# Performance work log

Hardware: AMD Instinct MI355X
Metric: run time of the kernel (lower is better)

## Reference

```python
import jax, jax.numpy as jnp
import numpy as np

B, T, S, D, H, E, K, FF = 4, 1024, 1024, 1024, 16, 8, 2, 4096
DH = D // H
EPS = 1e-5

def layernorm(x, g, b):
    m = x.mean(-1, keepdims=True)
    v = x.var(-1, keepdims=True)
    return (x - m) / jnp.sqrt(v + EPS) * g + b

def mha(q, k, v, mask, wq, bq, wk, bk, wv, bv, wo, bo):
    Bq, Tq, _ = q.shape
    Tk = k.shape[1]
    Q = (q @ wq + bq).reshape(Bq, Tq, H, DH).transpose(0, 2, 1, 3)
    Kh = (k @ wk + bk).reshape(Bq, Tk, H, DH).transpose(0, 2, 1, 3)
    V = (v @ wv + bv).reshape(Bq, Tk, H, DH).transpose(0, 2, 1, 3)
    scores = jnp.einsum('bhqd,bhkd->bhqk', Q, Kh) / (DH ** 0.5)
    scores = jnp.where(mask != 0, scores, jnp.float32(-1e9))
    A = jax.nn.softmax(scores, axis=-1)
    O = jnp.einsum('bhqk,bhkd->bhqd', A, V).transpose(0, 2, 1, 3).reshape(Bq, Tq, D)
    return O @ wo + bo

def sparse_moe(x, wg, bg, w1, b1, w2, b2):
    # x: [B,T,D] -> tokens [N,D]
    Bx, Tx, _ = x.shape
    xt = x.reshape(-1, D)
    N = xt.shape[0]
    probs = jax.nn.softmax(xt @ wg + bg, axis=-1)          # [N,E]
    topv, topi = jax.lax.top_k(probs, K)                    # [N,K]
    topv = topv / topv.sum(-1, keepdims=True)
    gates = jnp.zeros((N, E), xt.dtype).at[jnp.arange(N)[:, None], topi].set(topv)
    h = jax.nn.relu(jnp.einsum('nd,edh->enh', xt, w1) + b1[:, None, :])  # [E,N,FF]
    y = jnp.einsum('enh,ehd->end', h, w2) + b2[:, None, :]               # [E,N,D]
    out = jnp.einsum('ne,end->nd', gates, y)
    return out.reshape(Bx, Tx, D)

def setup_inputs() -> dict:
    key = jax.random.key(0)
    ks = jax.random.split(key, 32)
    r = lambda k, s: jax.random.normal(k, s, dtype=jnp.float32) * 0.02
    inp = {
        'x': jax.random.normal(ks[0], (B, T, D), jnp.float32),
        'encoder_out': jax.random.normal(ks[1], (B, S, D), jnp.float32),
        'src_attn_mask': jnp.ones((B, 1, 1, S), jnp.int32),
        'tgt_attn_mask': jnp.tril(jnp.ones((T, T), jnp.int32))[None, None],
        'ln1_g': jnp.ones((D,), jnp.float32), 'ln1_b': jnp.zeros((D,), jnp.float32),
        'ln2_g': jnp.ones((D,), jnp.float32), 'ln2_b': jnp.zeros((D,), jnp.float32),
        'ln3_g': jnp.ones((D,), jnp.float32), 'ln3_b': jnp.zeros((D,), jnp.float32),
        'wq1': r(ks[2], (D, D)), 'bq1': jnp.zeros((D,), jnp.float32),
        'wk1': r(ks[3], (D, D)), 'bk1': jnp.zeros((D,), jnp.float32),
        'wv1': r(ks[4], (D, D)), 'bv1': jnp.zeros((D,), jnp.float32),
        'wo1': r(ks[5], (D, D)), 'bo1': jnp.zeros((D,), jnp.float32),
        'wq2': r(ks[6], (D, D)), 'bq2': jnp.zeros((D,), jnp.float32),
        'wk2': r(ks[7], (D, D)), 'bk2': jnp.zeros((D,), jnp.float32),
        'wv2': r(ks[8], (D, D)), 'bv2': jnp.zeros((D,), jnp.float32),
        'wo2': r(ks[9], (D, D)), 'bo2': jnp.zeros((D,), jnp.float32),
        'wg': r(ks[10], (D, E)), 'bg': jnp.zeros((E,), jnp.float32),
        'w1': r(ks[11], (E, D, FF)), 'b1': jnp.zeros((E, FF), jnp.float32),
        'w2': r(ks[12], (E, FF, D)), 'b2': jnp.zeros((E, D), jnp.float32),
    }
    return inp

def reference(x, encoder_out, src_attn_mask, tgt_attn_mask,
              ln1_g, ln1_b, ln2_g, ln2_b, ln3_g, ln3_b,
              wq1, bq1, wk1, bk1, wv1, bv1, wo1, bo1,
              wq2, bq2, wk2, bk2, wv2, bv2, wo2, bo2,
              wg, bg, w1, b1, w2, b2):
    # pre-norm residual: x + sublayer(LN(x)); dropout=0 (eval)
    n1 = layernorm(x, ln1_g, ln1_b)
    h1 = x + mha(n1, n1, n1, tgt_attn_mask, wq1, bq1, wk1, bk1, wv1, bv1, wo1, bo1)
    n2 = layernorm(h1, ln2_g, ln2_b)
    h2 = h1 + mha(n2, encoder_out, encoder_out, src_attn_mask, wq2, bq2, wk2, bk2, wv2, bv2, wo2, bo2)
    n3 = layernorm(h2, ln3_g, ln3_b)
    h3 = h2 + sparse_moe(n3, wg, bg, w1, b1, w2, b2)
    return h3
```

## Files before the change

### kernel.cpp

```cpp
#include <hip/hip_runtime.h>

typedef unsigned short u16;
typedef float f32x4 __attribute__((ext_vector_type(4)));
typedef short s16x8 __attribute__((ext_vector_type(8)));
typedef u16   u16x4 __attribute__((ext_vector_type(4)));

#define DEV static __device__ __forceinline__

DEV u16 f2b(float f){
  unsigned u = __builtin_bit_cast(unsigned, f);
  u += 0x7fffu + ((u >> 16) & 1u);
  return (u16)(u >> 16);
}
DEV float b2f(u16 h){ unsigned u = ((unsigned)h) << 16; return __builtin_bit_cast(float, u); }
DEV void tsplit(float v, u16& hv, u16& lv){
  unsigned u = __builtin_bit_cast(unsigned, v);
  hv = (u16)(u >> 16);
  float rest = v - __builtin_bit_cast(float, u & 0xffff0000u);
  lv = (u16)(__builtin_bit_cast(unsigned, rest) >> 16);
}
DEV float fexp2(float x){ float r; asm("v_exp_f32 %0, %1" : "=v"(r) : "v"(x)); return r; }

DEV void glds16(const u16* g, u16* l){
  __builtin_amdgcn_global_load_lds(
      (const __attribute__((address_space(1))) void*)g,
      (__attribute__((address_space(3))) void*)l, 16, 0, 0);
}

DEV f32x4 mfma3(s16x8 ah, s16x8 al, s16x8 bh, s16x8 bl, f32x4 c){
  c = __builtin_amdgcn_mfma_f32_16x16x32_bf16(ah, bh, c, 0, 0, 0);
  c = __builtin_amdgcn_mfma_f32_16x16x32_bf16(ah, bl, c, 0, 0, 0);
  c = __builtin_amdgcn_mfma_f32_16x16x32_bf16(al, bh, c, 0, 0, 0);
  return c;
}

constexpr int TT = 1024, DM = 1024, NE = 8, FFD = 4096;
constexpr int NTOK = 4096;

struct Ptr8 { const float* p[8]; };

__global__ __launch_bounds__(256) void trans8_k(Ptr8 srcs, u16* __restrict__ dh, u16* __restrict__ dl){
  __shared__ float tl[64][65];
  const float* src = srcs.p[blockIdx.z];
  u16* dsth = dh + (size_t)blockIdx.z * 1024 * 1024;
  u16* dstl = dl + (size_t)blockIdx.z * 1024 * 1024;
  const int tid = threadIdx.x;
  const int r0 = blockIdx.y * 64, c0 = blockIdx.x * 64;
  const int ty = tid >> 4, tx = tid & 15;
#pragma unroll
  for (int i = 0; i < 4; i++){
    int row = ty + i * 16;
    f32x4 v = *(const f32x4*)&src[(size_t)(r0 + row) * 1024 + c0 + tx * 4];
#pragma unroll
    for (int j = 0; j < 4; j++) tl[row][tx * 4 + j] = v[j];
  }
  __syncthreads();
#pragma unroll
  for (int i = 0; i < 4; i++){
    int drow = ty + i * 16;
    u16x4 oh, ol;
#pragma unroll
    for (int j = 0; j < 4; j++){
      float v = tl[tx * 4 + j][drow];
      u16 hh, ll; tsplit(v, hh, ll);
      oh[j] = hh; ol[j] = ll;
    }
    *(u16x4*)&dsth[(size_t)(c0 + drow) * 1024 + r0 + tx * 4] = oh;
    *(u16x4*)&dstl[(size_t)(c0 + drow) * 1024 + r0 + tx * 4] = ol;
  }
}

__global__ __launch_bounds__(256) void transb_k(const float* __restrict__ src0, u16* __restrict__ dst0, int R, int C){
  __shared__ float tl[64][65];
  const float* src = src0 + (size_t)blockIdx.z * R * C;
  u16* dst = dst0 + (size_t)blockIdx.z * R * C;
  const int tid = threadIdx.x;
  const int r0 = blockIdx.y * 64, c0 = blockIdx.x * 64;
  const int ty = tid >> 4, tx = tid & 15;
#pragma unroll
  for (int i = 0; i < 4; i++){
    int row = ty + i * 16;
    f32x4 v = *(const f32x4*)&src[(size_t)(r0 + row) * C + c0 + tx * 4];
#pragma unroll
    for (int j = 0; j < 4; j++) tl[row][tx * 4 + j] = v[j];
  }
  __syncthreads();
#pragma unroll
  for (int i = 0; i < 4; i++){
    int drow = ty + i * 16;
    u16x4 o;
#pragma unroll
    for (int j = 0; j < 4; j++) o[j] = f2b(tl[tx * 4 + j][drow]);
    *(u16x4*)&dst[(size_t)(c0 + drow) * R + r0 + tx * 4] = o;
  }
}

__global__ __launch_bounds__(256) void split_k(const float* __restrict__ src,
                                               u16* __restrict__ dh, u16* __restrict__ dl, int n4){
  int i = blockIdx.x * 256 + threadIdx.x;
  if (i < n4){
    f32x4 v = *(const f32x4*)&src[(size_t)i * 4];
    u16x4 oh, ol;
#pragma unroll
    for (int j = 0; j < 4; j++){ u16 hh, ll; tsplit(v[j], hh, ll); oh[j] = hh; ol[j] = ll; }
    *(u16x4*)&dh[(size_t)i * 4] = oh;
    *(u16x4*)&dl[(size_t)i * 4] = ol;
  }
}

__global__ __launch_bounds__(256) void ln_k(const float* __restrict__ x, const float* __restrict__ g,
                                            const float* __restrict__ b,
                                            u16* __restrict__ outH, u16* __restrict__ outL){
  __shared__ float red[8];
  const int row = blockIdx.x, tid = threadIdx.x, l = tid & 63, wave = tid >> 6;
  f32x4 v = *(const f32x4*)&x[(size_t)row * DM + tid * 4];
  float s = v[0] + v[1] + v[2] + v[3];
  float sq = v[0]*v[0] + v[1]*v[1] + v[2]*v[2] + v[3]*v[3];
#pragma unroll
  for (int m = 1; m < 64; m <<= 1){ s += __shfl_xor(s, m); sq += __shfl_xor(sq, m); }
  if (l == 0){ red[wave] = s; red[4 + wave] = sq; }
  __syncthreads();
  float tot = red[0] + red[1] + red[2] + red[3];
  float totq = red[4] + red[5] + red[6] + red[7];
  float mean = tot * (1.0f / DM);
  float var = totq * (1.0f / DM) - mean * mean;
  float rstd = rsqrtf(var + 1e-5f);
  f32x4 gg = *(const f32x4*)&g[tid * 4];
  f32x4 bb = *(const f32x4*)&b[tid * 4];
  u16x4 oh, ol;
#pragma unroll
  for (int j = 0; j < 4; j++){
    float y = (v[j] - mean) * rstd * gg[j] + bb[j];
    u16 hh, ll; tsplit(y, hh, ll); oh[j] = hh; ol[j] = ll;
  }
  *(u16x4*)&outH[(size_t)row * DM + tid * 4] = oh;
  if (outL) *(u16x4*)&outL[(size_t)row * DM + tid * 4] = ol;
}

struct QKVArgs {
  const u16* ah[3]; const u16* al[3]; const float* bias[3];
};

__global__ __launch_bounds__(256) void gemm_qkv3_k(
    QKVArgs args, const u16* __restrict__ Bhp, const u16* __restrict__ Blp,
    u16* __restrict__ QH, u16* __restrict__ QL,
    u16* __restrict__ KH, u16* __restrict__ KL,
    u16* __restrict__ VTH, u16* __restrict__ VTL)
{
  constexpr int K = DM;
  __shared__ alignas(16) u16 LAh[128 * 32], LAl[128 * 32];
  __shared__ alignas(16) u16 LBh[64 * 32], LBl[64 * 32];
  const int tid = threadIdx.x, l = tid & 63, wave = tid >> 6;
  const int seg = blockIdx.z;
  const int m0 = blockIdx.y * 128, n0 = blockIdx.x * 64;
  const int r0 = tid >> 2, seg8 = (tid & 3) * 8;
  const u16* gAh = args.ah[seg] + (size_t)(m0 + r0) * K + seg8;
  const u16* gAl = args.al[seg] + (size_t)(m0 + r0) * K + seg8;
  const u16* gBh = Bhp + (size_t)(seg * 1024 + n0 + r0) * K + seg8;
  const u16* gBl = Blp + (size_t)(seg * 1024 + n0 + r0) * K + seg8;
  u16* wAh = &LAh[wave * 512]; u16* wAl = &LAl[wave * 512];
  u16* wBh = &LBh[wave * 512]; u16* wBl = &LBl[wave * 512];
  const size_t K64 = (size_t)64 * K;
  f32x4 acc[4][2];
#pragma unroll
  for (int i = 0; i < 4; i++)
#pragma unroll
    for (int j = 0; j < 2; j++) acc[i][j] = f32x4{0.f, 0.f, 0.f, 0.f};
  const int wm = (wave >> 1) * 64, wn = (wave & 1) * 32;
  for (int kt = 0; kt < K; kt += 32){
    __syncthreads();
    glds16(gAh + kt, wAh); glds16(gAh + kt + K64, wAh + 2048);
    glds16(gAl + kt, wAl); glds16(gAl + kt + K64, wAl + 2048);
    glds16(gBh + kt, wBh);
    glds16(gBl + kt, wBl);
    __syncthreads();
    s16x8 afh[4], afl[4], bfh[2], bfl[2];
#pragma unroll
    for (int i = 0; i < 4; i++){
      int ar = (wm + i * 16 + (l & 15)) * 32 + (l >> 4) * 8;
      afh[i] = *(const s16x8*)&LAh[ar];
      afl[i] = *(const s16x8*)&LAl[ar];
    }
#pragma unroll
    for (int j = 0; j < 2; j++){
      int br = (wn + j * 16 + (l & 15)) * 32 + (l >> 4) * 8;
      bfh[j] = *(const s16x8*)&LBh[br];
      bfl[j] = *(const s16x8*)&LBl[br];
    }
#pragma unroll
    for (int i = 0; i < 4; i++)
#pragma unroll
      for (int j = 0; j < 2; j++)
        acc[i][j] = mfma3(afh[i], afl[i], bfh[j], bfl[j], acc[i][j]);
  }
  const float* bp = args.bias[seg];
  u16* DH = (seg == 0) ? QH : KH;
  u16* DL = (seg == 0) ? QL : KL;
#pragma unroll
  for (int i = 0; i < 4; i++)
#pragma unroll
    for (int r = 0; r < 4; r++){
      int row = m0 + wm + i * 16 + (l >> 4) * 4 + r;
#pragma unroll
      for (int j = 0; j < 2; j++){
        int col = n0 + wn + j * 16 + (l & 15);
        float v = acc[i][j][r] + bp[col];
        u16 hv, lv; tsplit(v, hv, lv);
        if (seg == 2){
          int bb = row >> 10, tq = row & 1023, hh = col >> 6, dd = col & 63;
          size_t vi = ((size_t)((bb << 4) + hh) * 64 + dd) * 1024 + tq;
          VTH[vi] = hv; VTL[vi] = lv;
        } else {
          size_t idx = (size_t)row * 1024 + col;
          DH[idx] = hv; DL[idx] = lv;
        }
      }
    }
}

__global__ __launch_bounds__(256) void gemm_o64_k(
    const u16* __restrict__ Ahp, const u16* __restrict__ Alp,
    const u16* __restrict__ Bhp, const u16* __restrict__ Blp,
    const float* __restrict__ bias, const float* __restrict__ res,
    float* __restrict__ Cf)
{
  constexpr int K = DM;
  __shared__ alignas(16) u16 LAh[64 * 32], LAl[64 * 32];
  __shared__ alignas(16) u16 LBh[64 * 32], LBl[64 * 32];
  const int tid = threadIdx.x, l = tid & 63, wave = tid >> 6;
  const int m0 = blockIdx.y * 64, n0 = blockIdx.x * 64;
  const int rA = tid >> 2, seg8 = (tid & 3) * 8;
  const u16* gAh = Ahp + (size_t)(m0 + rA) * K + seg8;
  const u16* gAl = Alp + (size_t)(m0 + rA) * K + seg8;
  const u16* gBh = Bhp + (size_t)(n0 + rA) * K + seg8;
  const u16* gBl = Blp + (size_t)(n0 + rA) * K + seg8;
  u16* wAh = &LAh[wave * 512]; u16* wAl = &LAl[wave * 512];
  u16* wBh = &LBh[wave * 512]; u16* wBl = &LBl[wave * 512];
  f32x4 acc[2][2];
#pragma unroll
  for (int i = 0; i < 2; i++)
#pragma unroll
    for (int j = 0; j < 2; j++) acc[i][j] = f32x4{0.f, 0.f, 0.f, 0.f};
  const int wm = (wave >> 1) * 32, wn = (wave & 1) * 32;
  for (int kt = 0; kt < K; kt += 32){
    __syncthreads();
    glds16(gAh + kt, wAh);
    glds16(gAl + kt, wAl);
    glds16(gBh + kt, wBh);
    glds16(gBl + kt, wBl);
    __syncthreads();
    s16x8 afh[2], afl[2], bfh[2], bfl[2];
#pragma unroll
    for (int i = 0; i < 2; i++){
      int ar = (wm + i * 16 + (l & 15)) * 32 + (l >> 4) * 8;
      afh[i] = *(const s16x8*)&LAh[ar];
      afl[i] = *(const s16x8*)&LAl[ar];
    }
#pragma unroll
    for (int j = 0; j < 2; j++){
      int br = (wn + j * 16 + (l & 15)) * 32 + (l >> 4) * 8;
      bfh[j] = *(const s16x8*)&LBh[br];
      bfl[j] = *(const s16x8*)&LBl[br];
    }
#pragma unroll
    for (int i = 0; i < 2; i++)
#pragma unroll
      for (int j = 0; j < 2; j++)
        acc[i][j] = mfma3(afh[i], afl[i], bfh[j], bfl[j], acc[i][j]);
  }
#pragma unroll
  for (int i = 0; i < 2; i++)
#pragma unroll
    for (int r = 0; r < 4; r++){
      int row = m0 + wm + i * 16 + (l >> 4) * 4 + r;
#pragma unroll
      for (int j = 0; j < 2; j++){
        int col = n0 + wn + j * 16 + (l & 15);
        size_t idx = (size_t)row * 1024 + col;
        Cf[idx] = acc[i][j][r] + bias[col] + res[idx];
      }
    }
}

template<bool CAUSAL>
__global__ __launch_bounds__(512) void attn5_k(
    const u16* __restrict__ Qh, const u16* __restrict__ Ql,
    const u16* __restrict__ Kh, const u16* __restrict__ Kl,
    const u16* __restrict__ Vth, const u16* __restrict__ Vtl,
    const int* __restrict__ mask,
    float* __restrict__ OP0, float* __restrict__ OP1,
    float* __restrict__ LS0, float* __restrict__ LS1,
    int Tq, int Tk)
{
  constexpr float CS = 0.125f * 1.4426950408889634f;
  __shared__ alignas(16) u16 KhiL[2048], KloL[2048];
  __shared__ alignas(16) u16 VhiL[2048], VloL[2048];
  __shared__ alignas(16) u16 Plh[8][640], Pll[8][640];
  const int tid = threadIdx.x, l = tid & 63, wave = tid >> 6;
  const int id = blockIdx.x;
  const int bh = ((id >> 3) & 7) * 8 + (id & 7);
  const int b = bh >> 4, h = bh & 15;
  const int qt = (id >> 6) & 7, ks = id >> 9;
  const int q0 = qt * 128;
  float* __restrict__ OP = ks ? OP1 : OP0;
  float* __restrict__ LS = ks ? LS1 : LS0;
  const int ktBeg = ks * 512;
  int lim = CAUSAL ? (q0 + 128) : Tk;
  if (lim > Tk) lim = Tk;
  int ktEnd = (ks + 1) * 512;
  if (ktEnd > lim) ktEnd = lim;

  const int qr = q0 + wave * 16 + (l & 15);
  s16x8 qah[2], qal[2];
#pragma unroll
  for (int kb = 0; kb < 2; kb++){
    size_t base = (size_t)(b * Tq + qr) * DM + h * 64 + kb * 32 + (l >> 4) * 8;
    qah[kb] = *(const s16x8*)(Qh + base);
    qal[kb] = *(const s16x8*)(Ql + base);
  }

  const int sHalf = wave >> 2;
  const int sw = wave & 3;
  const int iS = sw * 64 + l;
  const int keyS = iS >> 3, cKS = iS & 7;
  const u16* gK = (sHalf ? Kl : Kh)
      + (size_t)(b * Tk + ktBeg + keyS) * DM + h * 64 + ((cKS ^ (keyS & 7)) * 8);
  u16* dK = (sHalf ? KloL : KhiL) + sw * 512;
  const int dS = iS >> 2, cVS = iS & 3;
  const size_t vgbase = (size_t)bh * 64 * 1024;
  const u16* gV = (sHalf ? Vtl : Vth)
      + vgbase + (size_t)dS * 1024 + ktBeg + ((cVS ^ ((dS >> 1) & 3)) * 8);
  u16* dV = (sHalf ? VloL : VhiL) + sw * 512;

  float lsum[4] = {0.f, 0.f, 0.f, 0.f};
  f32x4 oacc[4];
#pragma unroll
  for (int nb = 0; nb < 4; nb++) oacc[nb] = f32x4{0.f, 0.f, 0.f, 0.f};
  const int qgr = q0 + wave * 16 + (l >> 4) * 4;

  for (int kt = ktBeg; kt < ktEnd; kt += 32){
    __syncthreads();
    glds16(gK, dK); gK += (size_t)32 * DM;
    glds16(gV, dV); gV += 32;
    __syncthreads();

    f32x4 s[2];
#pragma unroll
    for (int n = 0; n < 2; n++){
      s[n] = f32x4{0.f, 0.f, 0.f, 0.f};
      const int key = n * 16 + (l & 15);
      const int sK = (key & 7);
#pragma unroll
      for (int kb = 0; kb < 2; kb++){
        const int cK = kb * 4 + (l >> 4);
        const int off = key * 64 + ((cK ^ sK) * 8);
        s16x8 kh = *(const s16x8*)&KhiL[off];
        s16x8 klo = *(const s16x8*)&KloL[off];
        s[n] = __builtin_amdgcn_mfma_f32_16x16x32_bf16(qah[kb], kh, s[n], 0, 0, 0);
        s[n] = __builtin_amdgcn_mfma_f32_16x16x32_bf16(qah[kb], klo, s[n], 0, 0, 0);
        s[n] = __builtin_amdgcn_mfma_f32_16x16x32_bf16(qal[kb], kh, s[n], 0, 0, 0);
      }
    }
    int key0 = kt + (l & 15), key1 = key0 + 16;
    int mv0 = 1, mv1 = 1;
    if (!CAUSAL && mask){ mv0 = mask[b * Tk + key0]; mv1 = mask[b * Tk + key1]; }
#pragma unroll
    for (int r = 0; r < 4; r++){
      float p0, p1;
      if (CAUSAL){
        int qg = qgr + r;
        p0 = (key0 <= qg) ? fexp2(s[0][r] * CS) : 0.f;
        p1 = (key1 <= qg) ? fexp2(s[1][r] * CS) : 0.f;
      } else {
        p0 = mv0 ? fexp2(s[0][r] * CS) : 0.f;
        p1 = mv1 ? fexp2(s[1][r] * CS) : 0.f;
      }
      lsum[r] += p0 + p1;
      int po = ((l >> 4) * 4 + r) * 40 + (l & 15);
      u16 h0, l0, h1, l1;
      tsplit(p0, h0, l0); tsplit(p1, h1, l1);
      Plh[wave][po] = h0;      Pll[wave][po] = l0;
      Plh[wave][po + 16] = h1; Pll[wave][po + 16] = l1;
    }
    s16x8 pah = *(const s16x8*)&Plh[wave][(l & 15) * 40 + (l >> 4) * 8];
    s16x8 pal = *(const s16x8*)&Pll[wave][(l & 15) * 40 + (l >> 4) * 8];
#pragma unroll
    for (int nb = 0; nb < 4; nb++){
      const int d = nb * 16 + (l & 15);
      const int off = d * 32 + (((l >> 4) ^ ((d >> 1) & 3)) * 8);
      s16x8 vfh = *(const s16x8*)&VhiL[off];
      s16x8 vfl = *(const s16x8*)&VloL[off];
      oacc[nb] = mfma3(pah, pal, vfh, vfl, oacc[nb]);
    }
  }
#pragma unroll
  for (int r = 0; r < 4; r++){
    float s = lsum[r];
    s += __shfl_xor(s, 1); s += __shfl_xor(s, 2);
    s += __shfl_xor(s, 4); s += __shfl_xor(s, 8);
    int qg = qgr + r;
    if ((l & 15) == 0) LS[(size_t)bh * 1024 + qg] = s;
#pragma unroll
    for (int nb = 0; nb < 4; nb++)
      OP[(size_t)(b * Tq + qg) * DM + h * 64 + nb * 16 + (l & 15)] = oacc[nb][r];
  }
}

__global__ __launch_bounds__(256) void norm_k(
    const float* __restrict__ OP0, const float* __restrict__ OP1,
    const float* __restrict__ LS0, const float* __restrict__ LS1,
    u16* __restrict__ Oh, u16* __restrict__ Ol)
{
  const int t = blockIdx.x, c = threadIdx.x * 4;
  const int b = t >> 10, q = t & 1023, h = c >> 6;
  const size_t li = (size_t)(b * 16 + h) * 1024 + q;
  float inv = 1.0f / (LS0[li] + LS1[li]);
  f32x4 o0 = *(const f32x4*)&OP0[(size_t)t * DM + c];
  f32x4 o1 = *(const f32x4*)&OP1[(size_t)t * DM + c];
  u16x4 oh, ol;
#pragma unroll
  for (int j = 0; j < 4; j++){
    float v = (o0[j] + o1[j]) * inv;
    u16 hh, ll; tsplit(v, hh, ll); oh[j] = hh; ol[j] = ll;
  }
  *(u16x4*)&Oh[(size_t)t * DM + c] = oh;
  *(u16x4*)&Ol[(size_t)t * DM + c] = ol;
}

__global__ __launch_bounds__(256) void moe_gate_k(const float* __restrict__ X,
    const float* __restrict__ g3, const float* __restrict__ b3,
    const float* __restrict__ wg, const float* __restrict__ bg,
    int* __restrict__ cnt, int* __restrict__ perm,
    int* __restrict__ toke, int* __restrict__ tokp, float* __restrict__ tokg)
{
  const int wave = threadIdx.x >> 6, l = threadIdx.x & 63;
  const int t = blockIdx.x * 4 + wave;
  float xv[16];
  float s = 0.f, sq = 0.f;
#pragma unroll
  for (int i = 0; i < 16; i++){
    xv[i] = X[(size_t)t * DM + l + i * 64];
    s += xv[i]; sq += xv[i] * xv[i];
  }
#pragma unroll
  for (int m = 1; m < 64; m <<= 1){ s += __shfl_xor(s, m); sq += __shfl_xor(sq, m); }
  float mean = s * (1.0f / DM);
  float var = sq * (1.0f / DM) - mean * mean;
  float rstd = rsqrtf(var + 1e-5f);
  float acc[8];
#pragma unroll
  for (int e = 0; e < 8; e++) acc[e] = 0.f;
#pragma unroll
  for (int i = 0; i < 16; i++){
    int k = l + i * 64;
    float xn = (xv[i] - mean) * rstd * g3[k] + b3[k];
    f32x4 wa = *(const f32x4*)&wg[k * 8];
    f32x4 wb = *(const f32x4*)&wg[k * 8 + 4];
#pragma unroll
    for (int j = 0; j < 4; j++){ acc[j] += xn * wa[j]; acc[4 + j] += xn * wb[j]; }
  }
#pragma unroll
  for (int e = 0; e < 8; e++)
#pragma unroll
    for (int m = 1; m < 64; m <<= 1) acc[e] += __shfl_xor(acc[e], m);
  if (l == 0){
    float lg[8];
#pragma unroll
    for (int e = 0; e < 8; e++) lg[e] = acc[e] + bg[e];
    float mx = lg[0];
#pragma unroll
    for (int e = 1; e < 8; e++) mx = fmaxf(mx, lg[e]);
    float ex[8]; float sum = 0.f;
#pragma unroll
    for (int e = 0; e < 8; e++){ ex[e] = expf(lg[e] - mx); sum += ex[e]; }
    int i0 = 0;
    for (int e = 1; e < 8; e++) if (ex[e] > ex[i0]) i0 = e;
    int i1 = (i0 == 0) ? 1 : 0;
    for (int e = 0; e < 8; e++) if (e != i0 && ex[e] > ex[i1]) i1 = e;
    float p0 = ex[i0] / sum, p1 = ex[i1] / sum;
    float gs = p0 + p1;
    int pos0 = atomicAdd(&cnt[i0], 1);
    int pos1 = atomicAdd(&cnt[i1], 1);
    perm[i0 * 4096 + pos0] = t;
    perm[i1 * 4096 + pos1] = t;
    toke[2 * t] = i0; toke[2 * t + 1] = i1;
    tokp[2 * t] = pos0; tokp[2 * t + 1] = pos1;
    tokg[2 * t] = p0 / gs; tokg[2 * t + 1] = p1 / gs;
  }
}

__global__ void offsets_k(const int* __restrict__ cnt, int* __restrict__ off){
  if (threadIdx.x == 0){
    int a = 0;
    for (int e = 0; e < 8; e++){ off[e] = a; a += cnt[e]; }
  }
}

__global__ __launch_bounds__(256) void gemm_moe1_k(
    const u16* __restrict__ X, const u16* __restrict__ W1t, const float* __restrict__ b1,
    const int* __restrict__ perm, const int* __restrict__ cnt, const int* __restrict__ off,
    u16* __restrict__ Hb)
{
  const int e = blockIdx.z;
  const int Ce = cnt[e];
  const int mt = blockIdx.y;
  if (mt * 128 >= Ce) return;
  __shared__ alignas(16) u16 Asl[2][128 * 32];
  __shared__ alignas(16) u16 Bsl[2][64 * 32];
  const int tid = threadIdx.x, l = tid & 63, wave = tid >> 6;
  const int n0 = blockIdx.x * 64;
  const int r0 = tid >> 2, seg = (tid & 3) * 8;
  const int rl0 = mt * 128 + r0, rl1 = rl0 + 64;
  const int g0 = perm[e * 4096 + (rl0 < Ce ? rl0 : Ce - 1)];
  const int g1 = perm[e * 4096 + (rl1 < Ce ? rl1 : Ce - 1)];
  const u16* gA0 = X + (size_t)g0 * DM + seg;
  const u16* gA1 = X + (size_t)g1 * DM + seg;
  const u16* gB = W1t + (size_t)e * FFD * DM + (size_t)(n0 + r0) * DM + seg;
  u16* wA0 = &Asl[0][wave * 512]; u16* wA1 = &Asl[1][wave * 512];
  u16* wB0 = &Bsl[0][wave * 512]; u16* wB1 = &Bsl[1][wave * 512];
  f32x4 acc[4][2];
#pragma unroll
  for (int i = 0; i < 4; i++)
#pragma unroll
    for (int j = 0; j < 2; j++) acc[i][j] = f32x4{0.f,0.f,0.f,0.f};
  const int wm = (wave >> 1) * 64, wn = (wave & 1) * 32;
  for (int kt = 0; kt < DM; kt += 64){
    __syncthreads();
    glds16(gA0 + kt, wA0);      glds16(gA1 + kt, wA0 + 2048);
    glds16(gA0 + kt + 32, wA1); glds16(gA1 + kt + 32, wA1 + 2048);
    glds16(gB + kt, wB0);
    glds16(gB + kt + 32, wB1);
    __syncthreads();
#pragma unroll
    for (int p = 0; p < 2; p++){
      s16x8 af[4], bfr[2];
#pragma unroll
      for (int i = 0; i < 4; i++)
        af[i]  = *(const s16x8*)&Asl[p][(wm + i * 16 + (l & 15)) * 32 + (l >> 4) * 8];
#pragma unroll
      for (int j = 0; j < 2; j++)
        bfr[j] = *(const s16x8*)&Bsl[p][(wn + j * 16 + (l & 15)) * 32 + (l >> 4) * 8];
#pragma unroll
      for (int i = 0; i < 4; i++)
#pragma unroll
        for (int j = 0; j < 2; j++)
          acc[i][j] = __builtin_amdgcn_mfma_f32_16x16x32_bf16(af[i], bfr[j], acc[i][j], 0, 0, 0);
    }
  }
  const int base = off[e];
#pragma unroll
  for (int i = 0; i < 4; i++)
#pragma unroll
    for (int r = 0; r < 4; r++){
      int rloc = mt * 128 + wm + i * 16 + (l >> 4) * 4 + r;
      if (rloc < Ce){
#pragma unroll
        for (int j = 0; j < 2; j++){
          int col = n0 + wn + j * 16 + (l & 15);
          float v = acc[i][j][r] + b1[e * FFD + col];
          v = fmaxf(v, 0.f);
          Hb[(size_t)(base + rloc) * FFD + col] = f2b(v);
        }
      }
    }
}

__global__ __launch_bounds__(512) void gemm_moe2_k(
    const u16* __restrict__ Hb, const u16* __restrict__ W2t,
    const int* __restrict__ cnt, const int* __restrict__ off, float* __restrict__ Y)
{
  const int id = blockIdx.x;
  const int e = id & 7;
  const int rest = id >> 3;
  const int n0 = (rest & 7) * 128;
  const int mt = rest >> 3;
  const int Ce = cnt[e];
  if (mt * 128 >= Ce) return;
  __shared__ alignas(16) u16 Asl[2][128 * 32];
  __shared__ alignas(16) u16 Bsl[2][128 * 32];
  const int tid = threadIdx.x, l = tid & 63, wave = tid >> 6;
  const int r0 = tid >> 2, seg = (tid & 3) * 8;
  const int base = off[e];
  const int rl = mt * 128 + r0;
  const int ar = base + (rl < Ce ? rl : Ce - 1);
  const u16* gA = Hb + (size_t)ar * FFD + seg;
  const u16* gB = W2t + (size_t)e * DM * FFD + (size_t)(n0 + r0) * FFD + seg;
  u16* wA0 = &Asl[0][wave * 512]; u16* wA1 = &Asl[1][wave * 512];
  u16* wB0 = &Bsl[0][wave * 512]; u16* wB1 = &Bsl[1][wave * 512];
  f32x4 acc[4][2];
#pragma unroll
  for (int i = 0; i < 4; i++)
#pragma unroll
    for (int j = 0; j < 2; j++) acc[i][j] = f32x4{0.f,0.f,0.f,0.f};
  const int wm = (wave >> 2) * 64, wn = (wave & 3) * 32;
  for (int kt = 0; kt < FFD; kt += 64){
    __syncthreads();
    glds16(gA + kt, wA0);
    glds16(gA + kt + 32, wA1);
    glds16(gB + kt, wB0);
    glds16(gB + kt + 32, wB1);
    __syncthreads();
#pragma unroll
    for (int p = 0; p < 2; p++){
      s16x8 af[4], bfr[2];
#pragma unroll
      for (int i = 0; i < 4; i++)
        af[i]  = *(const s16x8*)&Asl[p][(wm + i * 16 + (l & 15)) * 32 + (l >> 4) * 8];
#pragma unroll
      for (int j = 0; j < 2; j++)
        bfr[j] = *(const s16x8*)&Bsl[p][(wn + j * 16 + (l & 15)) * 32 + (l >> 4) * 8];
#pragma unroll
      for (int i = 0; i < 4; i++)
#pragma unroll
        for (int j = 0; j < 2; j++)
          acc[i][j] = __builtin_amdgcn_mfma_f32_16x16x32_bf16(af[i], bfr[j], acc[i][j], 0, 0, 0);
    }
  }
#pragma unroll
  for (int i = 0; i < 4; i++)
#pragma unroll
    for (int r = 0; r < 4; r++){
      int rloc = mt * 128 + wm + i * 16 + (l >> 4) * 4 + r;
      if (rloc < Ce){
#pragma unroll
        for (int j = 0; j < 2; j++){
          int col = n0 + wn + j * 16 + (l & 15);
          Y[(size_t)(base + rloc) * DM + col] = acc[i][j][r];
        }
      }
    }
}

__global__ __launch_bounds__(256) void combine_k(const float* __restrict__ h2,
    const float* __restrict__ Y,
    const int* __restrict__ toke, const int* __restrict__ tokp, const float* __restrict__ tokg,
    const int* __restrict__ off, const float* __restrict__ b2, float* __restrict__ out)
{
  const int t = blockIdx.x;
  const int c = threadIdx.x * 4;
  int e0 = toke[2 * t], e1 = toke[2 * t + 1];
  size_t r0 = (size_t)off[e0] + tokp[2 * t];
  size_t r1 = (size_t)off[e1] + tokp[2 * t + 1];
  float g0 = tokg[2 * t], g1 = tokg[2 * t + 1];
  f32x4 a  = *(const f32x4*)&h2[(size_t)t * DM + c];
  f32x4 y0 = *(const f32x4*)&Y[r0 * DM + c];
  f32x4 y1 = *(const f32x4*)&Y[r1 * DM + c];
  f32x4 v0 = *(const f32x4*)&b2[(size_t)e0 * DM + c];
  f32x4 v1 = *(const f32x4*)&b2[(size_t)e1 * DM + c];
  f32x4 o = a + (y0 + v0) * g0 + (y1 + v1) * g1;
  *(f32x4*)&out[(size_t)t * DM + c] = o;
}

extern "C" void kernel_launch(void* const* d_in, const int* in_sizes, int n_in,
                              void* d_out, int out_size, void* d_ws, size_t ws_size,
                              hipStream_t stream) {
  const float* x    = (const float*)d_in[0];
  const float* enc  = (const float*)d_in[1];
  const int* smask  = (const int*)d_in[2];
  const float* ln1g = (const float*)d_in[4]; const float* ln1b = (const float*)d_in[5];
  const float* ln2g = (const float*)d_in[6]; const float* ln2b = (const float*)d_in[7];
  const float* ln3g = (const float*)d_in[8]; const float* ln3b = (const float*)d_in[9];
  const float* wq1 = (const float*)d_in[10]; const float* bq1 = (const float*)d_in[11];
  const float* wk1 = (const float*)d_in[12]; const float* bk1 = (const float*)d_in[13];
  const float* wv1 = (const float*)d_in[14]; const float* bv1 = (const float*)d_in[15];
  const float* wo1 = (const float*)d_in[16]; const float* bo1 = (const float*)d_in[17];
  const float* wq2 = (const float*)d_in[18]; const float* bq2 = (const float*)d_in[19];
  const float* wk2 = (const float*)d_in[20]; const float* bk2 = (const float*)d_in[21];
  const float* wv2 = (const float*)d_in[22]; const float* bv2 = (const float*)d_in[23];
  const float* wo2 = (const float*)d_in[24]; const float* bo2 = (const float*)d_in[25];
  const float* wg  = (const float*)d_in[26]; const float* bg  = (const float*)d_in[27];
  const float* w1  = (const float*)d_in[28]; const float* b1  = (const float*)d_in[29];
  const float* w2  = (const float*)d_in[30]; const float* b2  = (const float*)d_in[31];

  const size_t MB = 1024ull * 1024ull;
  char* ws = (char*)d_ws;
  size_t o = 0;
  auto alloc = [&](size_t bytes) -> void* {
    void* p = ws + o;
    o += (bytes + 255) & ~(size_t)255;
    return p;
  };
  float* H1  = (float*)alloc(16 * MB);
  float* H2  = (float*)alloc(16 * MB);
  u16*  NBF  = (u16*) alloc(8 * MB);
  int* CNT  = (int*)alloc(256);
  int* OFF  = (int*)alloc(256);
  int* PERM = (int*)alloc((size_t)8 * 4096 * 4);
  int* TOKE = (int*)alloc((size_t)NTOK * 2 * 4);
  int* TOKP = (int*)alloc((size_t)NTOK * 2 * 4);
  float* TOKG = (float*)alloc((size_t)NTOK * 2 * 4);
  char* R = (char*)alloc(224 * MB);
  u16* WTH = (u16*)(R);
  u16* WTL = (u16*)(R + 16 * MB);
  u16* NH  = (u16*)(R + 32 * MB);
  u16* NL  = (u16*)(R + 40 * MB);
  u16* EH  = (u16*)(R + 48 * MB);
  u16* EL  = (u16*)(R + 56 * MB);
  u16* QH  = (u16*)(R + 64 * MB);
  u16* QL  = (u16*)(R + 72 * MB);
  u16* KH  = (u16*)(R + 80 * MB);
  u16* KL  = (u16*)(R + 88 * MB);
  u16* VTH = (u16*)(R + 96 * MB);
  u16* VTL = (u16*)(R + 104 * MB);
  u16* OH  = (u16*)(R + 112 * MB);
  u16* OL  = (u16*)(R + 120 * MB);
  float* OP0 = (float*)(R + 128 * MB);
  float* OP1 = (float*)(R + 144 * MB);
  float* LS0 = (float*)(R + 160 * MB);
  float* LS1 = (float*)(R + 161 * MB);
  u16* W1T = (u16*)(R);
  u16* W2T = (u16*)(R + 64 * MB);
  u16* HB  = (u16*)(R + 128 * MB);
  float* YB = (float*)(R + 192 * MB);

  Ptr8 p8; p8.p[0]=wq1; p8.p[1]=wk1; p8.p[2]=wv1; p8.p[3]=wo1;
           p8.p[4]=wq2; p8.p[5]=wk2; p8.p[6]=wv2; p8.p[7]=wo2;
  trans8_k<<<dim3(16,16,8), 256, 0, stream>>>(p8, WTH, WTL);
  split_k<<<dim3(4096), 256, 0, stream>>>(enc, EH, EL, NTOK * DM / 4);

  const size_t W = (size_t)1024 * 1024;
  ln_k<<<dim3(NTOK), 256, 0, stream>>>(x, ln1g, ln1b, NH, NL);
  {
    QKVArgs a;
    a.ah[0]=NH; a.ah[1]=NH; a.ah[2]=NH;
    a.al[0]=NL; a.al[1]=NL; a.al[2]=NL;
    a.bias[0]=bq1; a.bias[1]=bk1; a.bias[2]=bv1;
    gemm_qkv3_k<<<dim3(16,32,3), 256, 0, stream>>>(a, WTH + 0*W, WTL + 0*W,
                                                   QH, QL, KH, KL, VTH, VTL);
  }
  attn5_k<true><<<dim3(1024), 512, 0, stream>>>(QH, QL, KH, KL, VTH, VTL, nullptr,
                                                OP0, OP1, LS0, LS1, TT, TT);
  norm_k<<<dim3(NTOK), 256, 0, stream>>>(OP0, OP1, LS0, LS1, OH, OL);
  gemm_o64_k<<<dim3(16,64), 256, 0, stream>>>(OH, OL, WTH + 3*W, WTL + 3*W, bo1, x, H1);

  ln_k<<<dim3(NTOK), 256, 0, stream>>>(H1, ln2g, ln2b, NH, NL);
  {
    QKVArgs a;
    a.ah[0]=NH; a.ah[1]=EH; a.ah[2]=EH;
    a.al[0]=NL; a.al[1]=EL; a.al[2]=EL;
    a.bias[0]=bq2; a.bias[1]=bk2; a.bias[2]=bv2;
    gemm_qkv3_k<<<dim3(16,32,3), 256, 0, stream>>>(a, WTH + 4*W, WTL + 4*W,
                                                   QH, QL, KH, KL, VTH, VTL);
  }
  attn5_k<false><<<dim3(1024), 512, 0, stream>>>(QH, QL, KH, KL, VTH, VTL, smask,
                                                 OP0, OP1, LS0, LS1, TT, TT);
  norm_k<<<dim3(NTOK), 256, 0, stream>>>(OP0, OP1, LS0, LS1, OH, OL);
  gemm_o64_k<<<dim3(16,64), 256, 0, stream>>>(OH, OL, WTH + 7*W, WTL + 7*W, bo2, H1, H2);

  transb_k<<<dim3(64,16,8), 256, 0, stream>>>(w1, W1T, 1024, 4096);
  transb_k<<<dim3(16,64,8), 256, 0, stream>>>(w2, W2T, 4096, 1024);
  ln_k<<<dim3(NTOK), 256, 0, stream>>>(H2, ln3g, ln3b, NBF, nullptr);
  hipMemsetAsync(CNT, 0, 8 * sizeof(int), stream);
  moe_gate_k<<<dim3(1024), 256, 0, stream>>>(H2, ln3g, ln3b, wg, bg, CNT, PERM, TOKE, TOKP, TOKG);
  offsets_k<<<dim3(1), 64, 0, stream>>>(CNT, OFF);
  gemm_moe1_k<<<dim3(64,32,8), 256, 0, stream>>>(NBF, W1T, b1, PERM, CNT, OFF, HB);
  gemm_moe2_k<<<dim3(2048), 512, 0, stream>>>(HB, W2T, CNT, OFF, YB);
  combine_k<<<dim3(NTOK), 256, 0, stream>>>(H2, YB, TOKE, TOKP, TOKG, OFF, b2, (float*)d_out);
}
```

Measured before the change: 848.4 us.

## Enlarge QKV GEMM tile to 128x128 with 512 threads, K-step 64 and swizzled grid

The QKV projection GEMM now uses 128x128 output tiles computed by 8 waves instead of 128x64 by 4 waves. Each synchronisation round loads a 64-wide K slice into two LDS halves, which halves the number of barrier pairs. The grid becomes a flat 1D launch whose index is decoded so that neighbouring blocks share A rows across N tiles, improving L2 reuse. The cost is twice the LDS per block and larger blocks, which may lower occupancy, and there are fewer blocks to keep all CUs busy.

```diff
diff --git a/kernel.cpp b/kernel.cpp
--- a/kernel.cpp
+++ b/kernel.cpp
@@ -141,57 +141,62 @@
   const u16* ah[3]; const u16* al[3]; const float* bias[3];
 };
 
-__global__ __launch_bounds__(256) void gemm_qkv3_k(
+__global__ __launch_bounds__(512) void gemm_qkv3_k(
     QKVArgs args, const u16* __restrict__ Bhp, const u16* __restrict__ Blp,
     u16* __restrict__ QH, u16* __restrict__ QL,
     u16* __restrict__ KH, u16* __restrict__ KL,
     u16* __restrict__ VTH, u16* __restrict__ VTL)
 {
   constexpr int K = DM;
-  __shared__ alignas(16) u16 LAh[128 * 32], LAl[128 * 32];
-  __shared__ alignas(16) u16 LBh[64 * 32], LBl[64 * 32];
+  __shared__ alignas(16) u16 LAh[2][128 * 32], LAl[2][128 * 32];
+  __shared__ alignas(16) u16 LBh[2][128 * 32], LBl[2][128 * 32];
   const int tid = threadIdx.x, l = tid & 63, wave = tid >> 6;
-  const int seg = blockIdx.z;
-  const int m0 = blockIdx.y * 128, n0 = blockIdx.x * 64;
+  const int id = blockIdx.x;
+  const int mlo = id & 7, nb = (id >> 3) & 7, mhi = (id >> 6) & 3, seg = id >> 8;
+  const int m0 = (mlo + 8 * mhi) * 128, n0 = nb * 128;
   const int r0 = tid >> 2, seg8 = (tid & 3) * 8;
   const u16* gAh = args.ah[seg] + (size_t)(m0 + r0) * K + seg8;
   const u16* gAl = args.al[seg] + (size_t)(m0 + r0) * K + seg8;
   const u16* gBh = Bhp + (size_t)(seg * 1024 + n0 + r0) * K + seg8;
   const u16* gBl = Blp + (size_t)(seg * 1024 + n0 + r0) * K + seg8;
-  u16* wAh = &LAh[wave * 512]; u16* wAl = &LAl[wave * 512];
-  u16* wBh = &LBh[wave * 512]; u16* wBl = &LBl[wave * 512];
-  const size_t K64 = (size_t)64 * K;
+  u16* wAh0 = &LAh[0][wave * 512]; u16* wAh1 = &LAh[1][wave * 512];
+  u16* wAl0 = &LAl[0][wave * 512]; u16* wAl1 = &LAl[1][wave * 512];
+  u16* wBh0 = &LBh[0][wave * 512]; u16* wBh1 = &LBh[1][wave * 512];
+  u16* wBl0 = &LBl[0][wave * 512]; u16* wBl1 = &LBl[1][wave * 512];
   f32x4 acc[4][2];
 #pragma unroll
   for (int i = 0; i < 4; i++)
 #pragma unroll
     for (int j = 0; j < 2; j++) acc[i][j] = f32x4{0.f, 0.f, 0.f, 0.f};
-  const int wm = (wave >> 1) * 64, wn = (wave & 1) * 32;
-  for (int kt = 0; kt < K; kt += 32){
-    __syncthreads();
-    glds16(gAh + kt, wAh); glds16(gAh + kt + K64, wAh + 2048);
-    glds16(gAl + kt, wAl); glds16(gAl + kt + K64, wAl + 2048);
-    glds16(gBh + kt, wBh);
-    glds16(gBl + kt, wBl);
-    __syncthreads();
-    s16x8 afh[4], afl[4], bfh[2], bfl[2];
-#pragma unroll
-    for (int i = 0; i < 4; i++){
-      int ar = (wm + i * 16 + (l & 15)) * 32 + (l >> 4) * 8;
-      afh[i] = *(const s16x8*)&LAh[ar];
-      afl[i] = *(const s16x8*)&LAl[ar];
-    }
-#pragma unroll
-    for (int j = 0; j < 2; j++){
-      int br = (wn + j * 16 + (l & 15)) * 32 + (l >> 4) * 8;
-      bfh[j] = *(const s16x8*)&LBh[br];
-      bfl[j] = *(const s16x8*)&LBl[br];
-    }
-#pragma unroll
-    for (int i = 0; i < 4; i++)
-#pragma unroll
-      for (int j = 0; j < 2; j++)
-        acc[i][j] = mfma3(afh[i], afl[i], bfh[j], bfl[j], acc[i][j]);
+  const int wm = (wave >> 2) * 64, wn = (wave & 3) * 32;
+  for (int kt = 0; kt < K; kt += 64){
+    __syncthreads();
+    glds16(gAh + kt, wAh0); glds16(gAh + kt + 32, wAh1);
+    glds16(gAl + kt, wAl0); glds16(gAl + kt + 32, wAl1);
+    glds16(gBh + kt, wBh0); glds16(gBh + kt + 32, wBh1);
+    glds16(gBl + kt, wBl0); glds16(gBl + kt + 32, wBl1);
+    __syncthreads();
+#pragma unroll
+    for (int p = 0; p < 2; p++){
+      s16x8 afh[4], afl[4], bfh[2], bfl[2];
+#pragma unroll
+      for (int i = 0; i < 4; i++){
+        int ar = (wm + i * 16 + (l & 15)) * 32 + (l >> 4) * 8;
+        afh[i] = *(const s16x8*)&LAh[p][ar];
+        afl[i] = *(const s16x8*)&LAl[p][ar];
+      }
+#pragma unroll
+      for (int j = 0; j < 2; j++){
+        int br = (wn + j * 16 + (l & 15)) * 32 + (l >> 4) * 8;
+        bfh[j] = *(const s16x8*)&LBh[p][br];
+        bfl[j] = *(const s16x8*)&LBl[p][br];
+      }
+#pragma unroll
+      for (int i = 0; i < 4; i++)
+#pragma unroll
+        for (int j = 0; j < 2; j++)
+          acc[i][j] = mfma3(afh[i], afl[i], bfh[j], bfl[j], acc[i][j]);
+    }
   }
   const float* bp = args.bias[seg];
   u16* DH = (seg == 0) ? QH : KH;
@@ -725,8 +730,8 @@
     a.ah[0]=NH; a.ah[1]=NH; a.ah[2]=NH;
     a.al[0]=NL; a.al[1]=NL; a.al[2]=NL;
     a.bias[0]=bq1; a.bias[1]=bk1; a.bias[2]=bv1;
-    gemm_qkv3_k<<<dim3(16,32,3), 256, 0, stream>>>(a, WTH + 0*W, WTL + 0*W,
-                                                   QH, QL, KH, KL, VTH, VTL);
+    gemm_qkv3_k<<<dim3(768), 512, 0, stream>>>(a, WTH + 0*W, WTL + 0*W,
+                                               QH, QL, KH, KL, VTH, VTL);
   }
   attn5_k<true><<<dim3(1024), 512, 0, stream>>>(QH, QL, KH, KL, VTH, VTL, nullptr,
                                                 OP0, OP1, LS0, LS1, TT, TT);
@@ -739,8 +744,8 @@
     a.ah[0]=NH; a.ah[1]=EH; a.ah[2]=EH;
     a.al[0]=NL; a.al[1]=EL; a.al[2]=EL;
     a.bias[0]=bq2; a.bias[1]=bk2; a.bias[2]=bv2;
-    gemm_qkv3_k<<<dim3(16,32,3), 256, 0, stream>>>(a, WTH + 4*W, WTL + 4*W,
-                                                   QH, QL, KH, KL, VTH, VTL);
+    gemm_qkv3_k<<<dim3(768), 512, 0, stream>>>(a, WTH + 4*W, WTL + 4*W,
+                                               QH, QL, KH, KL, VTH, VTL);
   }
   attn5_k<false><<<dim3(1024), 512, 0, stream>>>(QH, QL, KH, KL, VTH, VTL, smask,
                                                  OP0, OP1, LS0, LS1, TT, TT);
```

After: 821.6 us. 1.03x faster.
